# Optimization experiments

Hardware: AMD Instinct MI355X
Metric: run time of the kernel (lower is better)

## Reference

```python
import jax, jax.numpy as jnp
import numpy as np

B, V, D, L = 2048, 50000, 256, 32
N = V - 1  # internal (non-leaf) Huffman nodes


def setup_inputs() -> dict:
    key = jax.random.key(0)
    k1, k2, k3, k4, k5, k6 = jax.random.split(key, 6)
    inputs_vector = jax.random.normal(k1, (B, V), jnp.float32)
    W = jax.random.normal(k2, (D, V), jnp.float32) / np.float32(np.sqrt(V))  # Linear weight [out,in]
    cls_w = jax.random.normal(k3, (N, D), jnp.float32)
    path_nodes = jax.random.randint(k4, (B, L), 0, N)
    huffman_codes = jax.random.randint(k5, (B, L), 0, 2).astype(jnp.int32)
    path_lengths = jax.random.randint(k6, (B,), 0, L).astype(jnp.int32)
    return {
        "inputs_vector": inputs_vector,
        "W": W,
        "cls_w": cls_w,
        "path_nodes": path_nodes,
        "huffman_codes": huffman_codes,
        "path_lengths": path_lengths,
    }


def reference(inputs_vector, W, cls_w, path_nodes, huffman_codes, path_lengths):
    # x = embedding(inputs_vector): Linear with no bias -> inputs @ W.T  [B, D]
    x = inputs_vector @ W.T
    # gather ragged Huffman-path node vectors (padded to L)  [B, L, D]
    path_vecs = cls_w[path_nodes]
    # per-sample tiny matmul: logits[i] = x[i] @ path_vecs[i].T  [B, L]
    logits = jnp.einsum("bd,bld->bl", x, path_vecs)
    y = huffman_codes.astype(logits.dtype)
    # stable BCE-with-logits per element
    bce = jnp.maximum(logits, 0.0) - logits * y + jnp.log1p(jnp.exp(-jnp.abs(logits)))
    # mask padded positions; per-sample mean over true path length (BCEWithLogitsLoss mean reduction)
    lengths = jnp.maximum(path_lengths, 1).astype(logits.dtype)  # guard length-0 pads
    mask = (jnp.arange(L)[None, :] < jnp.maximum(path_lengths, 1)[:, None]).astype(logits.dtype)
    per_sample = jnp.sum(bce * mask, axis=1) / lengths
    # loop accumulates per-sample means then divides by batch_size -> mean over batch
    loss = jnp.mean(per_sample)
    return loss[None]  # original returns a shape-[1] tensor
```

## Files before the change

### kernel.cpp

```cpp
#include <hip/hip_runtime.h>
#include <hip/hip_bf16.h>

#define M_DIM 2048
#define K_DIM 50000
#define N_DIM 256
#define L_PATH 32
#define BMt 128
#define BNt 256
#define BKt 64
#define TOTAL_KSTEPS 782
#define KSPLIT 16
#define STEPS_PER_SPLIT 49
#define MTILES 16

typedef __bf16 bf16x8 __attribute__((ext_vector_type(8)));
typedef __bf16 bf16x4 __attribute__((ext_vector_type(4)));
typedef float f32x4 __attribute__((ext_vector_type(4)));
typedef float fx4 __attribute__((ext_vector_type(4)));

__global__ __launch_bounds__(512)
void gemm_bf16_splitk(const float* __restrict__ A, const float* __restrict__ W,
                      float* __restrict__ outp, int use_atomic)
{
  __shared__ __align__(16) unsigned short sA[2][BMt * BKt];
  __shared__ __align__(16) unsigned short sW[2][BNt * BKt];

  int bid = blockIdx.x;
  int per = gridDim.x >> 3;
  int Lw = (bid & 7) * per + (bid >> 3);
  int mtile = Lw & (MTILES - 1);
  int ksp = Lw >> 4;

  int m0 = mtile * BMt;
  int s0 = ksp * STEPS_PER_SPLIT;
  int s1 = s0 + STEPS_PER_SPLIT;
  if (s1 > TOTAL_KSTEPS) s1 = TOTAL_KSTEPS;

  int tid = threadIdx.x;
  int wid = tid >> 6, lane = tid & 63;
  int wm = wid >> 2, wn = wid & 3;
  int l15 = lane & 15, l4 = lane >> 4;

  int rowt = tid >> 4;
  int chk  = tid & 15;
  const float* Ab = A + (size_t)(m0 + rowt) * K_DIM + chk * 4;
  const float* Wb = W + (size_t)rowt * K_DIM + chk * 4;

  int offA[4], offW[8];
#pragma unroll
  for (int i = 0; i < 4; ++i) {
    int r = i * 32 + rowt;
    offA[i] = r * BKt + ((((chk >> 1) ^ (r & 7)) << 3) + (chk & 1) * 4);
  }
#pragma unroll
  for (int i = 0; i < 8; ++i) {
    int r = i * 32 + rowt;
    offW[i] = r * BKt + ((((chk >> 1) ^ (r & 7)) << 3) + (chk & 1) * 4);
  }

  fx4 ra[4], rw[8];

  auto issue = [&](int s) {
    size_t kb = (size_t)s * BKt;
    const float* ap = Ab + kb;
    const float* wp = Wb + kb;
    int k = s * BKt + chk * 4;
    if (k + 4 <= K_DIM) {
#pragma unroll
      for (int i = 0; i < 4; ++i) ra[i] = *reinterpret_cast<const fx4*>(ap + (size_t)i * 32 * K_DIM);
#pragma unroll
      for (int i = 0; i < 8; ++i) rw[i] = *reinterpret_cast<const fx4*>(wp + (size_t)i * 32 * K_DIM);
    } else {
#pragma unroll
      for (int i = 0; i < 4; ++i) {
        fx4 f;
#pragma unroll
        for (int e = 0; e < 4; ++e) f[e] = (k + e < K_DIM) ? ap[(size_t)i * 32 * K_DIM + e] : 0.f;
        ra[i] = f;
      }
#pragma unroll
      for (int i = 0; i < 8; ++i) {
        fx4 f;
#pragma unroll
        for (int e = 0; e < 4; ++e) f[e] = (k + e < K_DIM) ? wp[(size_t)i * 32 * K_DIM + e] : 0.f;
        rw[i] = f;
      }
    }
  };

  auto pack = [&](int p) {
#pragma unroll
    for (int i = 0; i < 4; ++i) {
      bf16x4 h;
      h[0] = (__bf16)ra[i][0]; h[1] = (__bf16)ra[i][1];
      h[2] = (__bf16)ra[i][2]; h[3] = (__bf16)ra[i][3];
      *reinterpret_cast<bf16x4*>(&sA[p][offA[i]]) = h;
    }
#pragma unroll
    for (int i = 0; i < 8; ++i) {
      bf16x4 h;
      h[0] = (__bf16)rw[i][0]; h[1] = (__bf16)rw[i][1];
      h[2] = (__bf16)rw[i][2]; h[3] = (__bf16)rw[i][3];
      *reinterpret_cast<bf16x4*>(&sW[p][offW[i]]) = h;
    }
  };

  f32x4 acc[4][4] = {};

  auto compute = [&](int p) {
#pragma unroll
    for (int kk = 0; kk < 2; ++kk) {
      bf16x8 afr[4], bfr[4];
      int c = kk * 32 + l4 * 8;
#pragma unroll
      for (int mf = 0; mf < 4; ++mf) {
        int r = wm * 64 + mf * 16 + l15;
        afr[mf] = *reinterpret_cast<const bf16x8*>(&sA[p][r * BKt + (c ^ ((r & 7) << 3))]);
      }
#pragma unroll
      for (int nf = 0; nf < 4; ++nf) {
        int r = wn * 64 + nf * 16 + l15;
        bfr[nf] = *reinterpret_cast<const bf16x8*>(&sW[p][r * BKt + (c ^ ((r & 7) << 3))]);
      }
#pragma unroll
      for (int mf = 0; mf < 4; ++mf)
#pragma unroll
        for (int nf = 0; nf < 4; ++nf)
          acc[mf][nf] = __builtin_amdgcn_mfma_f32_16x16x32_bf16(afr[mf], bfr[nf], acc[mf][nf], 0, 0, 0);
    }
  };

#define WB() do { asm volatile("s_waitcnt lgkmcnt(0)" ::: "memory"); \
                  __builtin_amdgcn_s_barrier(); } while (0)

  issue(s0);
  pack(0);
  if (s0 + 1 < s1) issue(s0 + 1);
  WB();

  int p = 0;
  for (int t = s0; t < s1; ++t) {
    compute(p);
    if (t + 1 < s1) {
      pack(p ^ 1);
      if (t + 2 < s1) issue(t + 2);
      WB();
    }
    p ^= 1;
  }
#undef WB

  if (use_atomic) {
#pragma unroll
    for (int mf = 0; mf < 4; ++mf)
#pragma unroll
      for (int nf = 0; nf < 4; ++nf)
#pragma unroll
        for (int j = 0; j < 4; ++j) {
          int row = m0 + wm * 64 + mf * 16 + l4 * 4 + j;
          int col = wn * 64 + nf * 16 + l15;
          atomicAdd(&outp[(size_t)row * N_DIM + col], acc[mf][nf][j]);
        }
  } else {
    float* part = outp + (size_t)ksp * (M_DIM * N_DIM);
#pragma unroll
    for (int mf = 0; mf < 4; ++mf)
#pragma unroll
      for (int nf = 0; nf < 4; ++nf)
#pragma unroll
        for (int j = 0; j < 4; ++j) {
          int row = m0 + wm * 64 + mf * 16 + l4 * 4 + j;
          int col = wn * 64 + nf * 16 + l15;
          part[(size_t)row * N_DIM + col] = acc[mf][nf][j];
        }
  }
}

__global__ __launch_bounds__(256)
void loss_kernel(const float* __restrict__ part, int nparts,
                 const float* __restrict__ cls_w,
                 const int* __restrict__ nodes, const int* __restrict__ codes,
                 const int* __restrict__ lens, float* __restrict__ per_sample)
{
  int i = blockIdx.x;
  int tid = threadIdx.x;
  __shared__ float s_x[N_DIM];
  {
    float s = 0.f;
    for (int k = 0; k < nparts; ++k)
      s += part[(size_t)k * (M_DIM * N_DIM) + (size_t)i * N_DIM + tid];
    s_x[tid] = s;
  }
  __syncthreads();

  int wid = tid >> 6, lane = tid & 63;
  __shared__ float s_logit[L_PATH];
  fx4 xv = *reinterpret_cast<const fx4*>(&s_x[lane * 4]);
#pragma unroll
  for (int j = 0; j < 8; ++j) {
    int pos = wid * 8 + j;
    int node = nodes[i * L_PATH + pos];
    fx4 cv = *reinterpret_cast<const fx4*>(&cls_w[(size_t)node * N_DIM + lane * 4]);
    float d = xv[0] * cv[0] + xv[1] * cv[1] + xv[2] * cv[2] + xv[3] * cv[3];
#pragma unroll
    for (int s = 32; s > 0; s >>= 1) d += __shfl_xor(d, s);
    if (lane == 0) s_logit[pos] = d;
  }
  __syncthreads();
  if (wid == 0) {
    int len = lens[i];
    int lenc = len < 1 ? 1 : len;
    float v = 0.f;
    if (lane < L_PATH && lane < lenc) {
      float z = s_logit[lane];
      float y = (float)codes[i * L_PATH + lane];
      v = fmaxf(z, 0.f) - z * y + log1pf(expf(-fabsf(z)));
    }
#pragma unroll
    for (int s = 32; s > 0; s >>= 1) v += __shfl_xor(v, s);
    if (lane == 0) per_sample[i] = v / (float)lenc;
  }
}

__global__ __launch_bounds__(256)
void final_reduce(const float* __restrict__ ps, float* __restrict__ out) {
  int tid = threadIdx.x;
  float s = 0.f;
#pragma unroll
  for (int i = 0; i < M_DIM / 256; ++i) s += ps[tid + i * 256];
  __shared__ float sm[4];
#pragma unroll
  for (int sh = 32; sh > 0; sh >>= 1) s += __shfl_xor(s, sh);
  if ((tid & 63) == 0) sm[tid >> 6] = s;
  __syncthreads();
  if (tid == 0) out[0] = (sm[0] + sm[1] + sm[2] + sm[3]) * (1.0f / (float)M_DIM);
}

extern "C" void kernel_launch(void* const* d_in, const int* in_sizes, int n_in,
                              void* d_out, int out_size, void* d_ws, size_t ws_size,
                              hipStream_t stream) {
  const float* A     = (const float*)d_in[0];
  const float* W     = (const float*)d_in[1];
  const float* cls_w = (const float*)d_in[2];
  const int* nodes   = (const int*)d_in[3];
  const int* codes   = (const int*)d_in[4];
  const int* lens    = (const int*)d_in[5];
  float* out = (float*)d_out;

  char* ws = (char*)d_ws;
  const size_t XBYTES = (size_t)M_DIM * N_DIM * sizeof(float);
  float* per_sample = (float*)ws;
  float* x          = (float*)(ws + (size_t)(64u << 10));
  float* partials   = (float*)(ws + (size_t)(4u << 20));

  int use_atomic = (ws_size < (size_t)(4u << 20) + (size_t)KSPLIT * XBYTES) ? 1 : 0;

  if (use_atomic) {
    hipMemsetAsync(x, 0, XBYTES, stream);
    gemm_bf16_splitk<<<dim3(MTILES * KSPLIT), dim3(512), 0, stream>>>(A, W, x, 1);
    loss_kernel<<<dim3(M_DIM), dim3(256), 0, stream>>>(x, 1, cls_w, nodes, codes, lens, per_sample);
  } else {
    gemm_bf16_splitk<<<dim3(MTILES * KSPLIT), dim3(512), 0, stream>>>(A, W, partials, 0);
    loss_kernel<<<dim3(M_DIM), dim3(256), 0, stream>>>(partials, KSPLIT, cls_w, nodes, codes, lens, per_sample);
  }
  final_reduce<<<dim3(1), dim3(256), 0, stream>>>(per_sample, out);
}
```

Before: 153.5 us.

## Pre-convert W to swizzled bf16 tiles and stream via global_load_lds

```diff
diff --git a/kernel.cpp b/kernel.cpp
--- a/kernel.cpp
+++ b/kernel.cpp
@@ -12,18 +12,49 @@
 #define KSPLIT 16
 #define STEPS_PER_SPLIT 49
 #define MTILES 16
+#define WTILE_SHORTS (BNt * BKt)
 
 typedef __bf16 bf16x8 __attribute__((ext_vector_type(8)));
 typedef __bf16 bf16x4 __attribute__((ext_vector_type(4)));
+typedef __bf16 bf16x2 __attribute__((ext_vector_type(2)));
 typedef float f32x4 __attribute__((ext_vector_type(4)));
 typedef float fx4 __attribute__((ext_vector_type(4)));
 
+#define GLL(g, l) __builtin_amdgcn_global_load_lds(                        \
+    (const __attribute__((address_space(1))) void*)(g),                    \
+    (__attribute__((address_space(3))) void*)(l), 16, 0, 0)
+
+__global__ __launch_bounds__(256)
+void conv_w(const float* __restrict__ W, unsigned short* __restrict__ wsz)
+{
+  int s = blockIdx.x;
+  int tid = threadIdx.x;
+  int w = tid >> 6, lane = tid & 63;
+  int rl = lane >> 5;
+  int l31 = lane & 31;
+  int g = l31 >> 2, e2 = l31 & 3;
+  int kk = s * BKt + g * 8 + e2 * 2;
+  unsigned short* outs = wsz + (size_t)s * WTILE_SHORTS;
+#pragma unroll 4
+  for (int i = 0; i < 32; ++i) {
+    int r = i * 8 + w * 2 + rl;
+    bf16x2 hh;
+    if (kk + 2 <= K_DIM) {
+      const float* p = W + (size_t)r * K_DIM + kk;
+      hh[0] = (__bf16)p[0]; hh[1] = (__bf16)p[1];
+    } else {
+      hh[0] = (__bf16)0.f; hh[1] = (__bf16)0.f;
+    }
+    *reinterpret_cast<bf16x2*>(&outs[r * 64 + ((g ^ (r & 7)) * 8) + e2 * 2]) = hh;
+  }
+}
+
 __global__ __launch_bounds__(512)
-void gemm_bf16_splitk(const float* __restrict__ A, const float* __restrict__ W,
-                      float* __restrict__ outp, int use_atomic)
+void gemm_wpre(const float* __restrict__ A, const unsigned short* __restrict__ wsz,
+               float* __restrict__ outp, int use_atomic)
 {
   __shared__ __align__(16) unsigned short sA[2][BMt * BKt];
-  __shared__ __align__(16) unsigned short sW[2][BNt * BKt];
+  __shared__ __align__(16) unsigned short sW[3][WTILE_SHORTS];
 
   int bid = blockIdx.x;
   int per = gridDim.x >> 3;
@@ -44,22 +75,161 @@
   int rowt = tid >> 4;
   int chk  = tid & 15;
   const float* Ab = A + (size_t)(m0 + rowt) * K_DIM + chk * 4;
-  const float* Wb = W + (size_t)rowt * K_DIM + chk * 4;
-
-  int offA[4], offW[8];
+  int offA[4];
 #pragma unroll
   for (int i = 0; i < 4; ++i) {
     int r = i * 32 + rowt;
     offA[i] = r * BKt + ((((chk >> 1) ^ (r & 7)) << 3) + (chk & 1) * 4);
   }
+  fx4 ra[4];
+
+  auto issueA = [&](int s) {
+    size_t kb = (size_t)s * BKt;
+    const float* ap = Ab + kb;
+    if (s != TOTAL_KSTEPS - 1) {
+#pragma unroll
+      for (int i = 0; i < 4; ++i) ra[i] = *reinterpret_cast<const fx4*>(ap + (size_t)i * 32 * K_DIM);
+    } else {
+      int k = s * BKt + chk * 4;
+#pragma unroll
+      for (int i = 0; i < 4; ++i) {
+        fx4 f;
+#pragma unroll
+        for (int e = 0; e < 4; ++e) f[e] = (k + e < K_DIM) ? ap[(size_t)i * 32 * K_DIM + e] : 0.f;
+        ra[i] = f;
+      }
+    }
+  };
+
+  auto packA = [&](int p) {
+#pragma unroll
+    for (int i = 0; i < 4; ++i) {
+      bf16x4 h;
+      h[0] = (__bf16)ra[i][0]; h[1] = (__bf16)ra[i][1];
+      h[2] = (__bf16)ra[i][2]; h[3] = (__bf16)ra[i][3];
+      *reinterpret_cast<bf16x4*>(&sA[p][offA[i]]) = h;
+    }
+  };
+
+  const unsigned short* Wsrc = wsz + wid * 2048 + lane * 8;
+  auto gllW = [&](int t, int b) {
+    const unsigned short* src = Wsrc + (size_t)t * WTILE_SHORTS;
+    unsigned short* dst = &sW[b][wid * 2048];
+#pragma unroll
+    for (int c = 0; c < 4; ++c)
+      GLL(src + c * 512, dst + c * 512);
+  };
+
+  f32x4 acc[4][4] = {};
+
+  auto compute = [&](int pc, int bw) {
+#pragma unroll
+    for (int kk = 0; kk < 2; ++kk) {
+      bf16x8 afr[4], bfr[4];
+      int c = kk * 32 + l4 * 8;
+#pragma unroll
+      for (int mf = 0; mf < 4; ++mf) {
+        int r = wm * 64 + mf * 16 + l15;
+        afr[mf] = *reinterpret_cast<const bf16x8*>(&sA[pc][r * BKt + (c ^ ((r & 7) << 3))]);
+      }
+#pragma unroll
+      for (int nf = 0; nf < 4; ++nf) {
+        int r = wn * 64 + nf * 16 + l15;
+        bfr[nf] = *reinterpret_cast<const bf16x8*>(&sW[bw][r * BKt + (c ^ ((r & 7) << 3))]);
+      }
+#pragma unroll
+      for (int mf = 0; mf < 4; ++mf)
+#pragma unroll
+        for (int nf = 0; nf < 4; ++nf)
+          acc[mf][nf] = __builtin_amdgcn_mfma_f32_16x16x32_bf16(afr[mf], bfr[nf], acc[mf][nf], 0, 0, 0);
+    }
+  };
+
+  issueA(s0);
+  gllW(s0, 0);
+  packA(0);
+  issueA(s0 + 1);
+  gllW(s0 + 1, 1);
+  asm volatile("s_waitcnt lgkmcnt(0)" ::: "memory");
+  __builtin_amdgcn_s_barrier();
+
+  int t = s0;
+  for (; t < s1 - 1; ++t) {
+    int pc = (t - s0) & 1;
+    int bw = (t - s0) % 3;
+    asm volatile("s_waitcnt vmcnt(8)" ::: "memory");
+    compute(pc, bw);
+    packA(pc ^ 1);
+    if (t + 2 < s1) {
+      issueA(t + 2);
+      gllW(t + 2, (t - s0 + 2) % 3);
+    }
+    asm volatile("s_waitcnt lgkmcnt(0)" ::: "memory");
+    __builtin_amdgcn_s_barrier();
+  }
+  asm volatile("s_waitcnt vmcnt(0)" ::: "memory");
+  compute((t - s0) & 1, (t - s0) % 3);
+
+  if (use_atomic) {
+#pragma unroll
+    for (int mf = 0; mf < 4; ++mf)
+#pragma unroll
+      for (int nf = 0; nf < 4; ++nf)
+#pragma unroll
+        for (int j = 0; j < 4; ++j) {
+          int row = m0 + wm * 64 + mf * 16 + l4 * 4 + j;
+          int col = wn * 64 + nf * 16 + l15;
+          atomicAdd(&outp[(size_t)row * N_DIM + col], acc[mf][nf][j]);
+        }
+  } else {
+    float* part = outp + (size_t)ksp * (M_DIM * N_DIM);
+#pragma unroll
+    for (int mf = 0; mf < 4; ++mf)
+#pragma unroll
+      for (int nf = 0; nf < 4; ++nf)
+#pragma unroll
+        for (int j = 0; j < 4; ++j) {
+          int row = m0 + wm * 64 + mf * 16 + l4 * 4 + j;
+          int col = wn * 64 + nf * 16 + l15;
+          part[(size_t)row * N_DIM + col] = acc[mf][nf][j];
+        }
+  }
+}
+
+__global__ __launch_bounds__(512)
+void gemm_legacy(const float* __restrict__ A, const float* __restrict__ W,
+                 float* __restrict__ outp)
+{
+  __shared__ __align__(16) unsigned short sA[2][BMt * BKt];
+  __shared__ __align__(16) unsigned short sW[2][BNt * BKt];
+  int bid = blockIdx.x;
+  int per = gridDim.x >> 3;
+  int Lw = (bid & 7) * per + (bid >> 3);
+  int mtile = Lw & (MTILES - 1);
+  int ksp = Lw >> 4;
+  int m0 = mtile * BMt;
+  int s0 = ksp * STEPS_PER_SPLIT;
+  int s1 = s0 + STEPS_PER_SPLIT;
+  if (s1 > TOTAL_KSTEPS) s1 = TOTAL_KSTEPS;
+  int tid = threadIdx.x;
+  int wid = tid >> 6, lane = tid & 63;
+  int wm = wid >> 2, wn = wid & 3;
+  int l15 = lane & 15, l4 = lane >> 4;
+  int rowt = tid >> 4, chk = tid & 15;
+  const float* Ab = A + (size_t)(m0 + rowt) * K_DIM + chk * 4;
+  const float* Wb = W + (size_t)rowt * K_DIM + chk * 4;
+  int offA[4], offW[8];
+#pragma unroll
+  for (int i = 0; i < 4; ++i) {
+    int r = i * 32 + rowt;
+    offA[i] = r * BKt + ((((chk >> 1) ^ (r & 7)) << 3) + (chk & 1) * 4);
+  }
 #pragma unroll
   for (int i = 0; i < 8; ++i) {
     int r = i * 32 + rowt;
     offW[i] = r * BKt + ((((chk >> 1) ^ (r & 7)) << 3) + (chk & 1) * 4);
   }
-
   fx4 ra[4], rw[8];
-
   auto issue = [&](int s) {
     size_t kb = (size_t)s * BKt;
     const float* ap = Ab + kb;
@@ -87,7 +257,6 @@
       }
     }
   };
-
   auto pack = [&](int p) {
 #pragma unroll
     for (int i = 0; i < 4; ++i) {
@@ -104,9 +273,7 @@
       *reinterpret_cast<bf16x4*>(&sW[p][offW[i]]) = h;
     }
   };
-
   f32x4 acc[4][4] = {};
-
   auto compute = [&](int p) {
 #pragma unroll
     for (int kk = 0; kk < 2; ++kk) {
@@ -129,15 +296,12 @@
           acc[mf][nf] = __builtin_amdgcn_mfma_f32_16x16x32_bf16(afr[mf], bfr[nf], acc[mf][nf], 0, 0, 0);
     }
   };
-
 #define WB() do { asm volatile("s_waitcnt lgkmcnt(0)" ::: "memory"); \
                   __builtin_amdgcn_s_barrier(); } while (0)
-
   issue(s0);
   pack(0);
   if (s0 + 1 < s1) issue(s0 + 1);
   WB();
-
   int p = 0;
   for (int t = s0; t < s1; ++t) {
     compute(p);
@@ -149,38 +313,23 @@
     p ^= 1;
   }
 #undef WB
-
-  if (use_atomic) {
-#pragma unroll
-    for (int mf = 0; mf < 4; ++mf)
-#pragma unroll
-      for (int nf = 0; nf < 4; ++nf)
-#pragma unroll
-        for (int j = 0; j < 4; ++j) {
-          int row = m0 + wm * 64 + mf * 16 + l4 * 4 + j;
-          int col = wn * 64 + nf * 16 + l15;
-          atomicAdd(&outp[(size_t)row * N_DIM + col], acc[mf][nf][j]);
-        }
-  } else {
-    float* part = outp + (size_t)ksp * (M_DIM * N_DIM);
-#pragma unroll
-    for (int mf = 0; mf < 4; ++mf)
-#pragma unroll
-      for (int nf = 0; nf < 4; ++nf)
-#pragma unroll
-        for (int j = 0; j < 4; ++j) {
-          int row = m0 + wm * 64 + mf * 16 + l4 * 4 + j;
-          int col = wn * 64 + nf * 16 + l15;
-          part[(size_t)row * N_DIM + col] = acc[mf][nf][j];
-        }
-  }
+#pragma unroll
+  for (int mf = 0; mf < 4; ++mf)
+#pragma unroll
+    for (int nf = 0; nf < 4; ++nf)
+#pragma unroll
+      for (int j = 0; j < 4; ++j) {
+        int row = m0 + wm * 64 + mf * 16 + l4 * 4 + j;
+        int col = wn * 64 + nf * 16 + l15;
+        atomicAdd(&outp[(size_t)row * N_DIM + col], acc[mf][nf][j]);
+      }
 }
 
 __global__ __launch_bounds__(256)
 void loss_kernel(const float* __restrict__ part, int nparts,
                  const float* __restrict__ cls_w,
                  const int* __restrict__ nodes, const int* __restrict__ codes,
-                 const int* __restrict__ lens, float* __restrict__ per_sample)
+                 const int* __restrict__ lens, float* __restrict__ out)
 {
   int i = blockIdx.x;
   int tid = threadIdx.x;
@@ -218,22 +367,8 @@
     }
 #pragma unroll
     for (int s = 32; s > 0; s >>= 1) v += __shfl_xor(v, s);
-    if (lane == 0) per_sample[i] = v / (float)lenc;
-  }
-}
-
-__global__ __launch_bounds__(256)
-void final_reduce(const float* __restrict__ ps, float* __restrict__ out) {
-  int tid = threadIdx.x;
-  float s = 0.f;
-#pragma unroll
-  for (int i = 0; i < M_DIM / 256; ++i) s += ps[tid + i * 256];
-  __shared__ float sm[4];
-#pragma unroll
-  for (int sh = 32; sh > 0; sh >>= 1) s += __shfl_xor(s, sh);
-  if ((tid & 63) == 0) sm[tid >> 6] = s;
-  __syncthreads();
-  if (tid == 0) out[0] = (sm[0] + sm[1] + sm[2] + sm[3]) * (1.0f / (float)M_DIM);
+    if (lane == 0) atomicAdd(out, v / (float)lenc * (1.0f / (float)M_DIM));
+  }
 }
 
 extern "C" void kernel_launch(void* const* d_in, const int* in_sizes, int n_in,
@@ -248,20 +383,30 @@
   float* out = (float*)d_out;
 
   char* ws = (char*)d_ws;
-  const size_t XBYTES = (size_t)M_DIM * N_DIM * sizeof(float);
-  float* per_sample = (float*)ws;
-  float* x          = (float*)(ws + (size_t)(64u << 10));
-  float* partials   = (float*)(ws + (size_t)(4u << 20));
-
-  int use_atomic = (ws_size < (size_t)(4u << 20) + (size_t)KSPLIT * XBYTES) ? 1 : 0;
-
-  if (use_atomic) {
+  const size_t XBYTES  = (size_t)M_DIM * N_DIM * sizeof(float);
+  const size_t WSZB    = (size_t)TOTAL_KSTEPS * WTILE_SHORTS * 2;
+  const size_t OFF_WSZ = (size_t)(4u << 20);
+  const size_t OFF_PRT = (size_t)(32u << 20);
+  float*          x        = (float*)(ws + (size_t)(64u << 10));
+  unsigned short* wsz      = (unsigned short*)(ws + OFF_WSZ);
+  float*          partials = (float*)(ws + OFF_PRT);
+
+  const size_t need_full = OFF_PRT + (size_t)KSPLIT * XBYTES;
+  const size_t need_mid  = OFF_WSZ + WSZB;
+
+  hipMemsetAsync(out, 0, sizeof(float) * out_size, stream);
+  if (ws_size >= need_full) {
+    conv_w<<<dim3(TOTAL_KSTEPS), dim3(256), 0, stream>>>(W, wsz);
+    gemm_wpre<<<dim3(MTILES * KSPLIT), dim3(512), 0, stream>>>(A, wsz, partials, 0);
+    loss_kernel<<<dim3(M_DIM), dim3(256), 0, stream>>>(partials, KSPLIT, cls_w, nodes, codes, lens, out);
+  } else if (ws_size >= need_mid) {
     hipMemsetAsync(x, 0, XBYTES, stream);
-    gemm_bf16_splitk<<<dim3(MTILES * KSPLIT), dim3(512), 0, stream>>>(A, W, x, 1);
-    loss_kernel<<<dim3(M_DIM), dim3(256), 0, stream>>>(x, 1, cls_w, nodes, codes, lens, per_sample);
+    conv_w<<<dim3(TOTAL_KSTEPS), dim3(256), 0, stream>>>(W, wsz);
+    gemm_wpre<<<dim3(MTILES * KSPLIT), dim3(512), 0, stream>>>(A, wsz, x, 1);
+    loss_kernel<<<dim3(M_DIM), dim3(256), 0, stream>>>(x, 1, cls_w, nodes, codes, lens, out);
   } else {
-    gemm_bf16_splitk<<<dim3(MTILES * KSPLIT), dim3(512), 0, stream>>>(A, W, partials, 0);
-    loss_kernel<<<dim3(M_DIM), dim3(256), 0, stream>>>(partials, KSPLIT, cls_w, nodes, codes, lens, per_sample);
-  }
-  final_reduce<<<dim3(1), dim3(256), 0, stream>>>(per_sample, out);
+    hipMemsetAsync(x, 0, XBYTES, stream);
+    gemm_legacy<<<dim3(MTILES * KSPLIT), dim3(512), 0, stream>>>(A, W, x);
+    loss_kernel<<<dim3(M_DIM), dim3(256), 0, stream>>>(x, 1, cls_w, nodes, codes, lens, out);
+  }
 }
```

Measured after the change: 178.2 us. 16.1% more time.

## Raise split-K to 32, single-buffer W smem, fuse final reduction via atomics

Applied to the files above, without the earlier changes.

```diff
diff --git a/kernel.cpp b/kernel.cpp
--- a/kernel.cpp
+++ b/kernel.cpp
@@ -9,8 +9,6 @@
 #define BNt 256
 #define BKt 64
 #define TOTAL_KSTEPS 782
-#define KSPLIT 16
-#define STEPS_PER_SPLIT 49
 #define MTILES 16
 
 typedef __bf16 bf16x8 __attribute__((ext_vector_type(8)));
@@ -20,21 +18,17 @@
 
 __global__ __launch_bounds__(512)
 void gemm_bf16_splitk(const float* __restrict__ A, const float* __restrict__ W,
-                      float* __restrict__ outp, int use_atomic)
+                      float* __restrict__ outp, int kmask, int kshift, int use_atomic)
 {
   __shared__ __align__(16) unsigned short sA[2][BMt * BKt];
-  __shared__ __align__(16) unsigned short sW[2][BNt * BKt];
+  __shared__ __align__(16) unsigned short sW[BNt * BKt];
 
   int bid = blockIdx.x;
-  int per = gridDim.x >> 3;
-  int Lw = (bid & 7) * per + (bid >> 3);
-  int mtile = Lw & (MTILES - 1);
-  int ksp = Lw >> 4;
-
+  int ksp = bid & kmask;
+  int mtile = bid >> kshift;
   int m0 = mtile * BMt;
-  int s0 = ksp * STEPS_PER_SPLIT;
-  int s1 = s0 + STEPS_PER_SPLIT;
-  if (s1 > TOTAL_KSTEPS) s1 = TOTAL_KSTEPS;
+  int s0 = (TOTAL_KSTEPS * ksp) >> kshift;
+  int s1 = (TOTAL_KSTEPS * (ksp + 1)) >> kshift;
 
   int tid = threadIdx.x;
   int wid = tid >> 6, lane = tid & 63;
@@ -88,7 +82,16 @@
     }
   };
 
-  auto pack = [&](int p) {
+  auto packW = [&]() {
+#pragma unroll
+    for (int i = 0; i < 8; ++i) {
+      bf16x4 h;
+      h[0] = (__bf16)rw[i][0]; h[1] = (__bf16)rw[i][1];
+      h[2] = (__bf16)rw[i][2]; h[3] = (__bf16)rw[i][3];
+      *reinterpret_cast<bf16x4*>(&sW[offW[i]]) = h;
+    }
+  };
+  auto packA = [&](int p) {
 #pragma unroll
     for (int i = 0; i < 4; ++i) {
       bf16x4 h;
@@ -96,13 +99,6 @@
       h[2] = (__bf16)ra[i][2]; h[3] = (__bf16)ra[i][3];
       *reinterpret_cast<bf16x4*>(&sA[p][offA[i]]) = h;
     }
-#pragma unroll
-    for (int i = 0; i < 8; ++i) {
-      bf16x4 h;
-      h[0] = (__bf16)rw[i][0]; h[1] = (__bf16)rw[i][1];
-      h[2] = (__bf16)rw[i][2]; h[3] = (__bf16)rw[i][3];
-      *reinterpret_cast<bf16x4*>(&sW[p][offW[i]]) = h;
-    }
   };
 
   f32x4 acc[4][4] = {};
@@ -120,7 +116,7 @@
 #pragma unroll
       for (int nf = 0; nf < 4; ++nf) {
         int r = wn * 64 + nf * 16 + l15;
-        bfr[nf] = *reinterpret_cast<const bf16x8*>(&sW[p][r * BKt + (c ^ ((r & 7) << 3))]);
+        bfr[nf] = *reinterpret_cast<const bf16x8*>(&sW[r * BKt + (c ^ ((r & 7) << 3))]);
       }
 #pragma unroll
       for (int mf = 0; mf < 4; ++mf)
@@ -130,25 +126,26 @@
     }
   };
 
-#define WB() do { asm volatile("s_waitcnt lgkmcnt(0)" ::: "memory"); \
-                  __builtin_amdgcn_s_barrier(); } while (0)
-
   issue(s0);
-  pack(0);
+  packW();
+  packA(0);
   if (s0 + 1 < s1) issue(s0 + 1);
-  WB();
+  asm volatile("s_waitcnt lgkmcnt(0)" ::: "memory");
+  __builtin_amdgcn_s_barrier();
 
   int p = 0;
   for (int t = s0; t < s1; ++t) {
     compute(p);
     if (t + 1 < s1) {
-      pack(p ^ 1);
+      __builtin_amdgcn_s_barrier();
+      packW();
+      packA(p ^ 1);
       if (t + 2 < s1) issue(t + 2);
-      WB();
+      asm volatile("s_waitcnt lgkmcnt(0)" ::: "memory");
+      __builtin_amdgcn_s_barrier();
     }
     p ^= 1;
   }
-#undef WB
 
   if (use_atomic) {
 #pragma unroll
@@ -180,7 +177,7 @@
 void loss_kernel(const float* __restrict__ part, int nparts,
                  const float* __restrict__ cls_w,
                  const int* __restrict__ nodes, const int* __restrict__ codes,
-                 const int* __restrict__ lens, float* __restrict__ per_sample)
+                 const int* __restrict__ lens, float* __restrict__ out)
 {
   int i = blockIdx.x;
   int tid = threadIdx.x;
@@ -218,22 +215,8 @@
     }
 #pragma unroll
     for (int s = 32; s > 0; s >>= 1) v += __shfl_xor(v, s);
-    if (lane == 0) per_sample[i] = v / (float)lenc;
-  }
-}
-
-__global__ __launch_bounds__(256)
-void final_reduce(const float* __restrict__ ps, float* __restrict__ out) {
-  int tid = threadIdx.x;
-  float s = 0.f;
-#pragma unroll
-  for (int i = 0; i < M_DIM / 256; ++i) s += ps[tid + i * 256];
-  __shared__ float sm[4];
-#pragma unroll
-  for (int sh = 32; sh > 0; sh >>= 1) s += __shfl_xor(s, sh);
-  if ((tid & 63) == 0) sm[tid >> 6] = s;
-  __syncthreads();
-  if (tid == 0) out[0] = (sm[0] + sm[1] + sm[2] + sm[3]) * (1.0f / (float)M_DIM);
+    if (lane == 0) atomicAdd(out, v / (float)lenc * (1.0f / (float)M_DIM));
+  }
 }
 
 extern "C" void kernel_launch(void* const* d_in, const int* in_sizes, int n_in,
@@ -249,19 +232,22 @@
 
   char* ws = (char*)d_ws;
   const size_t XBYTES = (size_t)M_DIM * N_DIM * sizeof(float);
-  float* per_sample = (float*)ws;
-  float* x          = (float*)(ws + (size_t)(64u << 10));
-  float* partials   = (float*)(ws + (size_t)(4u << 20));
-
-  int use_atomic = (ws_size < (size_t)(4u << 20) + (size_t)KSPLIT * XBYTES) ? 1 : 0;
-
-  if (use_atomic) {
+  float* x        = (float*)(ws + (size_t)(64u << 10));
+  float* partials = (float*)(ws + (size_t)(4u << 20));
+
+  const size_t need32 = (size_t)(4u << 20) + 32 * XBYTES;
+  const size_t need16 = (size_t)(4u << 20) + 16 * XBYTES;
+
+  hipMemsetAsync(out, 0, sizeof(float) * out_size, stream);
+  if (ws_size >= need32) {
+    gemm_bf16_splitk<<<dim3(MTILES * 32), dim3(512), 0, stream>>>(A, W, partials, 31, 5, 0);
+    loss_kernel<<<dim3(M_DIM), dim3(256), 0, stream>>>(partials, 32, cls_w, nodes, codes, lens, out);
+  } else if (ws_size >= need16) {
+    gemm_bf16_splitk<<<dim3(MTILES * 16), dim3(512), 0, stream>>>(A, W, partials, 15, 4, 0);
+    loss_kernel<<<dim3(M_DIM), dim3(256), 0, stream>>>(partials, 16, cls_w, nodes, codes, lens, out);
+  } else {
     hipMemsetAsync(x, 0, XBYTES, stream);
-    gemm_bf16_splitk<<<dim3(MTILES * KSPLIT), dim3(512), 0, stream>>>(A, W, x, 1);
-    loss_kernel<<<dim3(M_DIM), dim3(256), 0, stream>>>(x, 1, cls_w, nodes, codes, lens, per_sample);
-  } else {
-    gemm_bf16_splitk<<<dim3(MTILES * KSPLIT), dim3(512), 0, stream>>>(A, W, partials, 0);
-    loss_kernel<<<dim3(M_DIM), dim3(256), 0, stream>>>(partials, KSPLIT, cls_w, nodes, codes, lens, per_sample);
-  }
-  final_reduce<<<dim3(1), dim3(256), 0, stream>>>(per_sample, out);
+    gemm_bf16_splitk<<<dim3(MTILES * 16), dim3(512), 0, stream>>>(A, W, x, 15, 4, 1);
+    loss_kernel<<<dim3(M_DIM), dim3(256), 0, stream>>>(x, 1, cls_w, nodes, codes, lens, out);
+  }
 }
```

Result: slower. 214.9 us (+39.9%).
